# Kernel tuning notes

Measured on AMD Instinct MI355X. Metric: run time of the kernel, lower is better.

## Reference

```python
import jax, jax.numpy as jnp
import numpy as np

N = 50000      # nodes
E = 1600000    # edges
M = 2          # modalities
DIN, H1, LAT, DEC, HID, NC = 2000, 500, 128, 64, 64, 16
EPS = 1e-5


def setup_inputs() -> dict:
    key = jax.random.key(0)
    ks = jax.random.split(key, 24)
    s = 0.02
    return {
        "x": jax.random.normal(ks[0], (M, N, DIN), jnp.float32),
        "src": jax.random.randint(ks[1], (E,), 0, N, jnp.int32),
        "dst": jax.random.randint(ks[2], (E,), 0, N, jnp.int32),
        "W1": jax.random.normal(ks[3], (M, DIN, H1), jnp.float32) * s,
        "b1": jax.random.normal(ks[4], (M, H1), jnp.float32) * s,
        "g1": jax.random.uniform(ks[5], (M, H1), jnp.float32) + 0.5,
        "be1": jax.random.normal(ks[6], (M, H1), jnp.float32) * s,
        "m1": jax.random.normal(ks[7], (M, H1), jnp.float32) * s,
        "v1": jax.random.uniform(ks[8], (M, H1), jnp.float32) + 0.5,
        "W2": jax.random.normal(ks[9], (M, H1, LAT), jnp.float32) * s,
        "b2": jax.random.normal(ks[10], (M, LAT), jnp.float32) * s,
        "g2": jax.random.uniform(ks[11], (M, LAT), jnp.float32) + 0.5,
        "be2": jax.random.normal(ks[12], (M, LAT), jnp.float32) * s,
        "m2": jax.random.normal(ks[13], (M, LAT), jnp.float32) * s,
        "v2": jax.random.uniform(ks[14], (M, LAT), jnp.float32) + 0.5,
        "Wd": jax.random.normal(ks[15], (M, LAT, DEC), jnp.float32) * s,
        "bd": jax.random.normal(ks[16], (M, DEC), jnp.float32) * s,
        "Wg1": jax.random.normal(ks[17], (DEC, HID), jnp.float32) * s,
        "bg1": jax.random.normal(ks[18], (HID,), jnp.float32) * s,
        "Wg2": jax.random.normal(ks[19], (HID, NC), jnp.float32) * s,
        "bg2": jax.random.normal(ks[20], (NC,), jnp.float32) * s,
    }


def _bn(h, g, b, m, v):
    # inference-mode BatchNorm1d; params broadcast over [M, 1, F]
    return (h - m[:, None, :]) * jax.lax.rsqrt(v[:, None, :] + EPS) * g[:, None, :] + b[:, None, :]


def reference(x, src, dst, W1, b1, g1, be1, m1, v1, W2, b2, g2, be2, m2, v2,
              Wd, bd, Wg1, bg1, Wg2, bg2):
    # --- multi-modal encoders (dropout = identity at eval) ---
    h = jnp.einsum('mnd,mdh->mnh', x, W1) + b1[:, None, :]        # [M,N,500]
    h = _bn(h, g1, be1, m1, v1)
    h = jnp.einsum('mnh,mhl->mnl', h, W2) + b2[:, None, :]        # [M,N,LAT]
    h = _bn(h, g2, be2, m2, v2)
    dec = jnp.einsum('mnl,mld->mnd', h, Wd) + bd[:, None, :]      # [M,N,DEC]
    node_features = jnp.mean(dec, axis=0)                         # [N,DEC]

    # --- GraphConv (DGL norm='both'): D_out^{-1/2} on src, D_in^{-1/2} on dst ---
    ones = jnp.ones(src.shape[0], jnp.float32)
    deg_out = jax.ops.segment_sum(ones, src, num_segments=N)
    deg_in = jax.ops.segment_sum(ones, dst, num_segments=N)
    c_src = jax.lax.rsqrt(jnp.clip(deg_out, 1.0))[:, None]
    c_dst = jax.lax.rsqrt(jnp.clip(deg_in, 1.0))[:, None]

    def gconv(feat, W, b):
        msg = (feat * c_src)[src]                                 # [E,F]
        agg = jax.ops.segment_sum(msg, dst, num_segments=N)       # [N,F]
        return (agg * c_dst) @ W + b

    h = jax.nn.relu(gconv(node_features, Wg1, bg1))               # [N,HID]
    score = gconv(h, Wg2, bg2)                                    # [N,NC]
    return score
```

## Files before the change

### kernel.cpp

```cpp
#include <hip/hip_runtime.h>

#define NN 50000
#define EE 1600000
#define MM 2
#define DIN 2000
#define H1 500
#define LAT 128
#define DECF 64
#define KTOT (MM*DIN)
#define KSTEPS (KTOT/32)
#define NTILES (NN/16)
#define EPSBN 1e-5f

typedef float f32x4 __attribute__((ext_vector_type(4)));
typedef short short8v __attribute__((ext_vector_type(8)));

__device__ __forceinline__ unsigned int pkbf(float a, float b){
  unsigned int ua = __float_as_uint(a), ub = __float_as_uint(b);
  ua = (ua + 0x7FFFu + ((ua>>16)&1u)) >> 16;
  ub = (ub + 0x7FFFu + ((ub>>16)&1u)) & 0xFFFF0000u;
  return ua | ub;
}

__global__ __launch_bounds__(256) void prepA(const float* __restrict__ W2,const float* __restrict__ Wd,
                      const float* __restrict__ g2,const float* __restrict__ v2,
                      float* __restrict__ T){
  __shared__ float a2[LAT];
  int m = (blockIdx.x*4) / H1;
  if (threadIdx.x < LAT)
    a2[threadIdx.x] = g2[m*LAT+threadIdx.x]*rsqrtf(v2[m*LAT+threadIdx.x]+EPSBN);
  __syncthreads();
  int g = blockIdx.x*256 + threadIdx.x;
  int d = g & 63; int mk = g >> 6; int k = mk % H1;
  const float* w2 = W2 + (size_t)(m*H1 + k)*LAT;
  const float* wd = Wd + (size_t)m*LAT*DECF + d;
  float acc = 0.f;
  for (int l = 0; l < LAT; ++l) acc += w2[l]*a2[l]*wd[(size_t)l*DECF];
  T[g] = acc;
}

__global__ __launch_bounds__(256) void prepB(const float* __restrict__ W1,const float* __restrict__ g1,
                      const float* __restrict__ v1,const float* __restrict__ T,
                      unsigned short* __restrict__ WB){
  __shared__ float a1[H1];
  int m = (blockIdx.x*4) / DIN;
  for (int k = threadIdx.x; k < H1; k += 256)
    a1[k] = g1[m*H1+k]*rsqrtf(v1[m*H1+k]+EPSBN);
  __syncthreads();
  int g = blockIdx.x*256 + threadIdx.x;
  int d = g & 63; int mi = g >> 6; int i = mi % DIN;
  const float* w1 = W1 + (size_t)(m*DIN + i)*H1;
  const float* t  = T + (size_t)m*H1*DECF + d;
  float acc = 0.f;
  for (int k = 0; k < H1; ++k) acc += w1[k]*a1[k]*t[(size_t)k*DECF];
  acc *= 0.5f;
  unsigned int u = __float_as_uint(acc);
  unsigned short bf = (unsigned short)((u + 0x7FFFu + ((u>>16)&1u)) >> 16);
  int kc = m*DIN + i;
  int s = kc >> 5, kl = kc & 31;
  int laneB = ((kl>>3)<<4) | (d & 15);
  int t4 = d >> 4;
  WB[((size_t)((s*4 + t4)*64 + laneB))*8 + (kl & 7)] = bf;
}

__global__ void prepC(const float* __restrict__ b1,const float* __restrict__ g1,const float* __restrict__ be1,
                      const float* __restrict__ m1,const float* __restrict__ v1,
                      const float* __restrict__ b2,const float* __restrict__ g2,const float* __restrict__ be2,
                      const float* __restrict__ m2,const float* __restrict__ v2,
                      const float* __restrict__ T,const float* __restrict__ Wd,
                      const float* __restrict__ bd, float* __restrict__ cbar){
  __shared__ float part[128];
  int d = threadIdx.x & 63, h = threadIdx.x >> 6;
  float s = 0.f;
  for (int m = 0; m < MM; ++m){
    if (h == 0) s += bd[m*DECF + d];
    const float* t = T + (size_t)m*H1*DECF + d;
    for (int k = h*(H1/2); k < (h+1)*(H1/2); ++k){
      float a = g1[m*H1+k]*rsqrtf(v1[m*H1+k]+EPSBN);
      float c = (b1[m*H1+k]-m1[m*H1+k])*a + be1[m*H1+k];
      s += c*t[(size_t)k*DECF];
    }
    const float* wd = Wd + (size_t)m*LAT*DECF + d;
    for (int l = h*(LAT/2); l < (h+1)*(LAT/2); ++l){
      float a = g2[m*LAT+l]*rsqrtf(v2[m*LAT+l]+EPSBN);
      float c = (b2[m*LAT+l]-m2[m*LAT+l])*a + be2[m*LAT+l];
      s += c*wd[(size_t)l*DECF];
    }
  }
  part[threadIdx.x] = s;
  __syncthreads();
  if (h == 0) cbar[d] = 0.5f*(part[d] + part[64+d]);
}

__global__ void degk(const int* __restrict__ src,const int* __restrict__ dst,
                     int* __restrict__ dout,int* __restrict__ din){
  int e = blockIdx.x*blockDim.x + threadIdx.x;
  if (e >= EE) return;
  atomicAdd(&dout[src[e]], 1);
  atomicAdd(&din[dst[e]], 1);
}

__global__ __launch_bounds__(1024) void scan1(const int* __restrict__ deg, int* __restrict__ rp,
                      int* __restrict__ bsum, int n){
  __shared__ int sm[1024];
  int i = blockIdx.x*1024 + threadIdx.x;
  int v = (i < n) ? deg[i] : 0;
  sm[threadIdx.x] = v; __syncthreads();
  for (int off=1; off<1024; off<<=1){
    int t = (threadIdx.x >= off) ? sm[threadIdx.x-off] : 0;
    __syncthreads();
    sm[threadIdx.x] += t;
    __syncthreads();
  }
  if (i < n) rp[i] = sm[threadIdx.x] - v;
  if (threadIdx.x == 1023) bsum[blockIdx.x] = sm[1023];
}

__global__ void scan3n(int* __restrict__ rp, const int* __restrict__ bsum,
                       const int* __restrict__ dout, const int* __restrict__ din,
                       float* __restrict__ csrc, float* __restrict__ cdst){
  int i = blockIdx.x*blockDim.x + threadIdx.x;
  if (i >= NN) return;
  int b = i >> 10;
  int base = 0;
  for (int j = 0; j < b; ++j) base += bsum[j];
  rp[i] += base;
  if (i == NN-1) rp[NN] = EE;
  int a = dout[i]; if (a < 1) a = 1;
  int dd = din[i]; if (dd < 1) dd = 1;
  csrc[i] = rsqrtf((float)a);
  cdst[i] = rsqrtf((float)dd);
}

__global__ void scatk(const int* __restrict__ src,const int* __restrict__ dst,
                      const int* __restrict__ rp,int* __restrict__ cur,int* __restrict__ ss){
  int e = blockIdx.x*blockDim.x + threadIdx.x;
  if (e >= EE) return;
  int d = dst[e];
  int p = rp[d] + atomicAdd(&cur[d], 1);
  ss[p] = src[e];
}

__global__ __launch_bounds__(256) void gemm_nf(
    const float* __restrict__ x, const short8v* __restrict__ WB,
    const float* __restrict__ cbar, const float* __restrict__ csrc,
    float* __restrict__ nfpre, int* __restrict__ ticket)
{
  const int lane = threadIdx.x & 63;
  const int r = lane & 15;
  const int kg = (lane >> 4) << 3;
  const int rg = (lane >> 4) << 2;
  const float cb0 = cbar[r], cb1 = cbar[16+r], cb2 = cbar[32+r], cb3 = cbar[48+r];

  while (true){
    int t = 0;
    if (lane == 0) t = atomicAdd(ticket, 1);
    t = __shfl(t, 0, 64);
    if (t >= NTILES) break;
    const int n0 = t*16;
    const float* xrow = x + (size_t)(n0 + r) * DIN;

    f32x4 acc0 = {0.f,0.f,0.f,0.f}, acc1 = acc0, acc2 = acc0, acc3 = acc0;
    f32x4 A0c, A1c; short8v B0c, B1c, B2c, B3c;
    {
      const float* p = xrow + kg;
      A0c = *(const f32x4*)p; A1c = *(const f32x4*)(p+4);
      const short8v* bp = WB + lane;
      B0c = bp[0]; B1c = bp[64]; B2c = bp[128]; B3c = bp[192];
    }
    for (int s = 0; s < KSTEPS-1; ++s){
      f32x4 A0n, A1n; short8v B0n, B1n, B2n, B3n;
      {
        int kr = (s+1)*32 + kg;
        const float* p = (kr < DIN) ? (xrow + kr)
                                    : (xrow + (size_t)(NN-1)*DIN + kr);
        A0n = *(const f32x4*)p; A1n = *(const f32x4*)(p+4);
        const short8v* bp = WB + (size_t)(s+1)*256 + lane;
        B0n = bp[0]; B1n = bp[64]; B2n = bp[128]; B3n = bp[192];
      }
      union { short8v v; unsigned int u[4]; } AF;
      AF.u[0]=pkbf(A0c[0],A0c[1]); AF.u[1]=pkbf(A0c[2],A0c[3]);
      AF.u[2]=pkbf(A1c[0],A1c[1]); AF.u[3]=pkbf(A1c[2],A1c[3]);
      acc0 = __builtin_amdgcn_mfma_f32_16x16x32_bf16(AF.v, B0c, acc0, 0,0,0);
      acc1 = __builtin_amdgcn_mfma_f32_16x16x32_bf16(AF.v, B1c, acc1, 0,0,0);
      acc2 = __builtin_amdgcn_mfma_f32_16x16x32_bf16(AF.v, B2c, acc2, 0,0,0);
      acc3 = __builtin_amdgcn_mfma_f32_16x16x32_bf16(AF.v, B3c, acc3, 0,0,0);
      A0c=A0n; A1c=A1n; B0c=B0n; B1c=B1n; B2c=B2n; B3c=B3n;
    }
    {
      union { short8v v; unsigned int u[4]; } AF;
      AF.u[0]=pkbf(A0c[0],A0c[1]); AF.u[1]=pkbf(A0c[2],A0c[3]);
      AF.u[2]=pkbf(A1c[0],A1c[1]); AF.u[3]=pkbf(A1c[2],A1c[3]);
      acc0 = __builtin_amdgcn_mfma_f32_16x16x32_bf16(AF.v, B0c, acc0, 0,0,0);
      acc1 = __builtin_amdgcn_mfma_f32_16x16x32_bf16(AF.v, B1c, acc1, 0,0,0);
      acc2 = __builtin_amdgcn_mfma_f32_16x16x32_bf16(AF.v, B2c, acc2, 0,0,0);
      acc3 = __builtin_amdgcn_mfma_f32_16x16x32_bf16(AF.v, B3c, acc3, 0,0,0);
    }
    #pragma unroll
    for (int rr = 0; rr < 4; ++rr){
      int rowD = n0 + rg + rr;
      float cs = csrc[rowD];
      float* o = nfpre + (size_t)rowD*64 + r;
      o[0]  = (acc0[rr] + cb0)*cs;
      o[16] = (acc1[rr] + cb1)*cs;
      o[32] = (acc2[rr] + cb2)*cs;
      o[48] = (acc3[rr] + cb3)*cs;
    }
  }
}

__global__ __launch_bounds__(512) void fgd1(const float* __restrict__ nf,const int* __restrict__ rp,
                      const int* __restrict__ ss,const float* __restrict__ Wg1,
                      const float* __restrict__ bg1,const float* __restrict__ csrc,
                      const float* __restrict__ cdst,float* __restrict__ hpre){
  __shared__ float W[64*64];
  for (int i = threadIdx.x; i < 64*64; i += 512) W[i] = Wg1[i];
  __syncthreads();
  int wave = threadIdx.x >> 6, lane = threadIdx.x & 63;
  int n = blockIdx.x*8 + wave;
  int q = lane >> 4, c0 = (lane & 15)*4;
  int beg = rp[n], end = rp[n+1];
  f32x4 s4 = {0.f,0.f,0.f,0.f};
  int e = beg + q;
  for (; e + 12 < end; e += 16){
    int i0 = ss[e], i1 = ss[e+4], i2 = ss[e+8], i3 = ss[e+12];
    f32x4 f0 = *(const f32x4*)(nf + (size_t)i0*64 + c0);
    f32x4 f1 = *(const f32x4*)(nf + (size_t)i1*64 + c0);
    f32x4 f2 = *(const f32x4*)(nf + (size_t)i2*64 + c0);
    f32x4 f3 = *(const f32x4*)(nf + (size_t)i3*64 + c0);
    s4 += (f0 + f1) + (f2 + f3);
  }
  for (; e < end; e += 4)
    s4 += *(const f32x4*)(nf + (size_t)ss[e]*64 + c0);
  s4.x += __shfl_xor(s4.x,16); s4.y += __shfl_xor(s4.y,16);
  s4.z += __shfl_xor(s4.z,16); s4.w += __shfl_xor(s4.w,16);
  s4.x += __shfl_xor(s4.x,32); s4.y += __shfl_xor(s4.y,32);
  s4.z += __shfl_xor(s4.z,32); s4.w += __shfl_xor(s4.w,32);
  float acc = 0.f;
  #pragma unroll
  for (int l16 = 0; l16 < 16; ++l16){
    acc += __shfl(s4.x,l16) * W[(4*l16+0)*64 + lane];
    acc += __shfl(s4.y,l16) * W[(4*l16+1)*64 + lane];
    acc += __shfl(s4.z,l16) * W[(4*l16+2)*64 + lane];
    acc += __shfl(s4.w,l16) * W[(4*l16+3)*64 + lane];
  }
  float h = fmaxf(cdst[n]*acc + bg1[lane], 0.f) * csrc[n];
  hpre[(size_t)n*64 + lane] = h;
}

__global__ __launch_bounds__(512) void fgd2(const float* __restrict__ hp,const int* __restrict__ rp,
                      const int* __restrict__ ss,const float* __restrict__ Wg2,
                      const float* __restrict__ bg2,const float* __restrict__ cdst,
                      float* __restrict__ score){
  __shared__ float W[64*16];
  for (int i = threadIdx.x; i < 64*16; i += 512) W[i] = Wg2[i];
  __syncthreads();
  int wave = threadIdx.x >> 6, lane = threadIdx.x & 63;
  int n = blockIdx.x*8 + wave;
  int q = lane >> 4, c0 = (lane & 15)*4;
  int beg = rp[n], end = rp[n+1];
  f32x4 s4 = {0.f,0.f,0.f,0.f};
  int e = beg + q;
  for (; e + 12 < end; e += 16){
    int i0 = ss[e], i1 = ss[e+4], i2 = ss[e+8], i3 = ss[e+12];
    f32x4 f0 = *(const f32x4*)(hp + (size_t)i0*64 + c0);
    f32x4 f1 = *(const f32x4*)(hp + (size_t)i1*64 + c0);
    f32x4 f2 = *(const f32x4*)(hp + (size_t)i2*64 + c0);
    f32x4 f3 = *(const f32x4*)(hp + (size_t)i3*64 + c0);
    s4 += (f0 + f1) + (f2 + f3);
  }
  for (; e < end; e += 4)
    s4 += *(const f32x4*)(hp + (size_t)ss[e]*64 + c0);
  s4.x += __shfl_xor(s4.x,16); s4.y += __shfl_xor(s4.y,16);
  s4.z += __shfl_xor(s4.z,16); s4.w += __shfl_xor(s4.w,16);
  s4.x += __shfl_xor(s4.x,32); s4.y += __shfl_xor(s4.y,32);
  s4.z += __shfl_xor(s4.z,32); s4.w += __shfl_xor(s4.w,32);
  int c = lane & 15;
  float acc = 0.f;
  #pragma unroll
  for (int l16 = 0; l16 < 16; ++l16){
    acc += __shfl(s4.x,l16) * W[(4*l16+0)*16 + c];
    acc += __shfl(s4.y,l16) * W[(4*l16+1)*16 + c];
    acc += __shfl(s4.z,l16) * W[(4*l16+2)*16 + c];
    acc += __shfl(s4.w,l16) * W[(4*l16+3)*16 + c];
  }
  if (lane < 16) score[(size_t)n*16 + lane] = cdst[n]*acc + bg2[lane];
}

extern "C" void kernel_launch(void* const* d_in, const int* in_sizes, int n_in,
                              void* d_out, int out_size, void* d_ws, size_t ws_size,
                              hipStream_t stream){
  const float* x   = (const float*)d_in[0];
  const int* src   = (const int*)d_in[1];
  const int* dst   = (const int*)d_in[2];
  const float* W1  = (const float*)d_in[3];
  const float* b1  = (const float*)d_in[4];
  const float* g1  = (const float*)d_in[5];
  const float* be1 = (const float*)d_in[6];
  const float* m1  = (const float*)d_in[7];
  const float* v1  = (const float*)d_in[8];
  const float* W2  = (const float*)d_in[9];
  const float* b2  = (const float*)d_in[10];
  const float* g2  = (const float*)d_in[11];
  const float* be2 = (const float*)d_in[12];
  const float* m2  = (const float*)d_in[13];
  const float* v2  = (const float*)d_in[14];
  const float* Wd  = (const float*)d_in[15];
  const float* bd  = (const float*)d_in[16];
  const float* Wg1 = (const float*)d_in[17];
  const float* bg1 = (const float*)d_in[18];
  const float* Wg2 = (const float*)d_in[19];
  const float* bg2 = (const float*)d_in[20];
  float* score = (float*)d_out;

  char* w = (char*)d_ws;
  size_t off = 0;
  auto alc = [&](size_t b){ size_t c = off; off += (b + 255) & ~(size_t)255; return c; };
  size_t o_dout = alc((size_t)NN*4), o_din = alc((size_t)NN*4), o_cur = alc((size_t)NN*4);
  size_t o_tick = alc(256);
  size_t zspan = off;
  size_t o_rp  = alc((size_t)(NN+1)*4), o_bsum = alc(256*4);
  size_t o_csrc = alc((size_t)NN*4), o_cdst = alc((size_t)NN*4);
  size_t o_T = alc((size_t)MM*H1*DECF*4), o_cbar = alc(DECF*4);
  size_t o_WB = alc((size_t)MM*DIN*DECF*2);
  size_t o_ss = alc((size_t)EE*4);
  size_t o_nf = alc((size_t)NN*64*4);
  size_t o_hp = alc((size_t)NN*64*4);

  int* dout = (int*)(w+o_dout); int* din = (int*)(w+o_din); int* cur = (int*)(w+o_cur);
  int* tick = (int*)(w+o_tick);
  int* rp = (int*)(w+o_rp); int* bsum = (int*)(w+o_bsum);
  float* csrc = (float*)(w+o_csrc); float* cdst = (float*)(w+o_cdst);
  float* T = (float*)(w+o_T); float* cbar = (float*)(w+o_cbar);
  unsigned short* WBu = (unsigned short*)(w+o_WB);
  int* ss = (int*)(w+o_ss);
  float* nf = (float*)(w+o_nf); float* hp = (float*)(w+o_hp);

  hipMemsetAsync(w, 0, zspan, stream);

  prepA<<<(MM*H1*DECF)/256,256,0,stream>>>(W2,Wd,g2,v2,T);
  prepB<<<(MM*DIN*DECF)/256,256,0,stream>>>(W1,g1,v1,T,WBu);
  prepC<<<1,128,0,stream>>>(b1,g1,be1,m1,v1,b2,g2,be2,m2,v2,T,Wd,bd,cbar);

  degk<<<(EE+255)/256,256,0,stream>>>(src,dst,dout,din);
  int nb = (NN+1023)/1024;
  scan1<<<nb,1024,0,stream>>>(din,rp,bsum,NN);
  scan3n<<<(NN+255)/256,256,0,stream>>>(rp,bsum,dout,din,csrc,cdst);
  scatk<<<(EE+255)/256,256,0,stream>>>(src,dst,rp,cur,ss);

  gemm_nf<<<768,256,0,stream>>>(x,(const short8v*)(w+o_WB),cbar,csrc,nf,tick);

  fgd1<<<NN/8,512,0,stream>>>(nf,rp,ss,Wg1,bg1,csrc,cdst,hp);
  fgd2<<<NN/8,512,0,stream>>>(hp,rp,ss,Wg2,bg2,cdst,score);
}
```

Baseline: 797.4 us.

## Fuse degree counting into GEMM launch, store node features as bf16, persistent gconv

```diff
diff --git a/kernel.cpp b/kernel.cpp
--- a/kernel.cpp
+++ b/kernel.cpp
@@ -10,10 +10,13 @@
 #define KTOT (MM*DIN)
 #define KSTEPS (KTOT/32)
 #define NTILES (NN/16)
+#define GEMM_BLKS 768
+#define DEG_BLKS 256
 #define EPSBN 1e-5f
 
 typedef float f32x4 __attribute__((ext_vector_type(4)));
 typedef short short8v __attribute__((ext_vector_type(8)));
+typedef unsigned int u32x2 __attribute__((ext_vector_type(2)));
 
 __device__ __forceinline__ unsigned int pkbf(float a, float b){
   unsigned int ua = __float_as_uint(a), ub = __float_as_uint(b);
@@ -21,6 +24,12 @@
   ub = (ub + 0x7FFFu + ((ub>>16)&1u)) & 0xFFFF0000u;
   return ua | ub;
 }
+__device__ __forceinline__ unsigned short pk1(float a){
+  unsigned int u = __float_as_uint(a);
+  return (unsigned short)((u + 0x7FFFu + ((u>>16)&1u)) >> 16);
+}
+__device__ __forceinline__ float bfe0(unsigned int w){ return __uint_as_float(w<<16); }
+__device__ __forceinline__ float bfe1(unsigned int w){ return __uint_as_float(w & 0xFFFF0000u); }
 
 __global__ __launch_bounds__(256) void prepA(const float* __restrict__ W2,const float* __restrict__ Wd,
                       const float* __restrict__ g2,const float* __restrict__ v2,
@@ -92,14 +101,6 @@
   if (h == 0) cbar[d] = 0.5f*(part[d] + part[64+d]);
 }
 
-__global__ void degk(const int* __restrict__ src,const int* __restrict__ dst,
-                     int* __restrict__ dout,int* __restrict__ din){
-  int e = blockIdx.x*blockDim.x + threadIdx.x;
-  if (e >= EE) return;
-  atomicAdd(&dout[src[e]], 1);
-  atomicAdd(&din[dst[e]], 1);
-}
-
 __global__ __launch_bounds__(1024) void scan1(const int* __restrict__ deg, int* __restrict__ rp,
                       int* __restrict__ bsum, int n){
   __shared__ int sm[1024];
@@ -141,11 +142,21 @@
   ss[p] = src[e];
 }
 
-__global__ __launch_bounds__(256) void gemm_nf(
+__global__ __launch_bounds__(256,4) void gemm_deg(
     const float* __restrict__ x, const short8v* __restrict__ WB,
-    const float* __restrict__ cbar, const float* __restrict__ csrc,
-    float* __restrict__ nfpre, int* __restrict__ ticket)
+    const float* __restrict__ cbar,
+    unsigned short* __restrict__ nfb, int* __restrict__ ticket,
+    const int* __restrict__ src, const int* __restrict__ dst,
+    int* __restrict__ dout, int* __restrict__ din)
 {
+  if (blockIdx.x >= GEMM_BLKS){
+    int t0 = (blockIdx.x - GEMM_BLKS)*256 + threadIdx.x;
+    for (int e = t0; e < EE; e += 256*DEG_BLKS){
+      atomicAdd(&dout[src[e]], 1);
+      atomicAdd(&din[dst[e]], 1);
+    }
+    return;
+  }
   const int lane = threadIdx.x & 63;
   const int r = lane & 15;
   const int kg = (lane >> 4) << 3;
@@ -199,92 +210,110 @@
     #pragma unroll
     for (int rr = 0; rr < 4; ++rr){
       int rowD = n0 + rg + rr;
-      float cs = csrc[rowD];
-      float* o = nfpre + (size_t)rowD*64 + r;
-      o[0]  = (acc0[rr] + cb0)*cs;
-      o[16] = (acc1[rr] + cb1)*cs;
-      o[32] = (acc2[rr] + cb2)*cs;
-      o[48] = (acc3[rr] + cb3)*cs;
-    }
-  }
-}
-
-__global__ __launch_bounds__(512) void fgd1(const float* __restrict__ nf,const int* __restrict__ rp,
-                      const int* __restrict__ ss,const float* __restrict__ Wg1,
-                      const float* __restrict__ bg1,const float* __restrict__ csrc,
-                      const float* __restrict__ cdst,float* __restrict__ hpre){
+      unsigned short* o = nfb + (size_t)rowD*64 + r;
+      o[0]  = pk1(acc0[rr] + cb0);
+      o[16] = pk1(acc1[rr] + cb1);
+      o[32] = pk1(acc2[rr] + cb2);
+      o[48] = pk1(acc3[rr] + cb3);
+    }
+  }
+}
+
+__global__ __launch_bounds__(512,4) void fgd1(const unsigned short* __restrict__ nfb,
+                      const int* __restrict__ rp,const int* __restrict__ ss,
+                      const float* __restrict__ Wg1,const float* __restrict__ bg1,
+                      const float* __restrict__ csrc,const float* __restrict__ cdst,
+                      unsigned short* __restrict__ hpb){
   __shared__ float W[64*64];
   for (int i = threadIdx.x; i < 64*64; i += 512) W[i] = Wg1[i];
   __syncthreads();
   int wave = threadIdx.x >> 6, lane = threadIdx.x & 63;
-  int n = blockIdx.x*8 + wave;
-  int q = lane >> 4, c0 = (lane & 15)*4;
-  int beg = rp[n], end = rp[n+1];
-  f32x4 s4 = {0.f,0.f,0.f,0.f};
-  int e = beg + q;
-  for (; e + 12 < end; e += 16){
-    int i0 = ss[e], i1 = ss[e+4], i2 = ss[e+8], i3 = ss[e+12];
-    f32x4 f0 = *(const f32x4*)(nf + (size_t)i0*64 + c0);
-    f32x4 f1 = *(const f32x4*)(nf + (size_t)i1*64 + c0);
-    f32x4 f2 = *(const f32x4*)(nf + (size_t)i2*64 + c0);
-    f32x4 f3 = *(const f32x4*)(nf + (size_t)i3*64 + c0);
-    s4 += (f0 + f1) + (f2 + f3);
-  }
-  for (; e < end; e += 4)
-    s4 += *(const f32x4*)(nf + (size_t)ss[e]*64 + c0);
-  s4.x += __shfl_xor(s4.x,16); s4.y += __shfl_xor(s4.y,16);
-  s4.z += __shfl_xor(s4.z,16); s4.w += __shfl_xor(s4.w,16);
-  s4.x += __shfl_xor(s4.x,32); s4.y += __shfl_xor(s4.y,32);
-  s4.z += __shfl_xor(s4.z,32); s4.w += __shfl_xor(s4.w,32);
-  float acc = 0.f;
-  #pragma unroll
-  for (int l16 = 0; l16 < 16; ++l16){
-    acc += __shfl(s4.x,l16) * W[(4*l16+0)*64 + lane];
-    acc += __shfl(s4.y,l16) * W[(4*l16+1)*64 + lane];
-    acc += __shfl(s4.z,l16) * W[(4*l16+2)*64 + lane];
-    acc += __shfl(s4.w,l16) * W[(4*l16+3)*64 + lane];
-  }
-  float h = fmaxf(cdst[n]*acc + bg1[lane], 0.f) * csrc[n];
-  hpre[(size_t)n*64 + lane] = h;
-}
-
-__global__ __launch_bounds__(512) void fgd2(const float* __restrict__ hp,const int* __restrict__ rp,
-                      const int* __restrict__ ss,const float* __restrict__ Wg2,
-                      const float* __restrict__ bg2,const float* __restrict__ cdst,
-                      float* __restrict__ score){
+  int q = lane >> 4, cc = (lane & 15)*4;
+  const int NW = 512*8;
+  for (int n = blockIdx.x*8 + wave; n < NN; n += NW){
+    int beg = rp[n], end = rp[n+1];
+    f32x4 s4 = {0.f,0.f,0.f,0.f};
+    int e = beg + q;
+    for (; e + 12 < end; e += 16){
+      int i0 = ss[e], i1 = ss[e+4], i2 = ss[e+8], i3 = ss[e+12];
+      float c0 = csrc[i0], c1 = csrc[i1], c2 = csrc[i2], c3 = csrc[i3];
+      u32x2 w0 = *(const u32x2*)(nfb + (size_t)i0*64 + cc);
+      u32x2 w1 = *(const u32x2*)(nfb + (size_t)i1*64 + cc);
+      u32x2 w2 = *(const u32x2*)(nfb + (size_t)i2*64 + cc);
+      u32x2 w3 = *(const u32x2*)(nfb + (size_t)i3*64 + cc);
+      s4.x += c0*bfe0(w0.x) + c1*bfe0(w1.x) + c2*bfe0(w2.x) + c3*bfe0(w3.x);
+      s4.y += c0*bfe1(w0.x) + c1*bfe1(w1.x) + c2*bfe1(w2.x) + c3*bfe1(w3.x);
+      s4.z += c0*bfe0(w0.y) + c1*bfe0(w1.y) + c2*bfe0(w2.y) + c3*bfe0(w3.y);
+      s4.w += c0*bfe1(w0.y) + c1*bfe1(w1.y) + c2*bfe1(w2.y) + c3*bfe1(w3.y);
+    }
+    for (; e < end; e += 4){
+      int i0 = ss[e]; float c0 = csrc[i0];
+      u32x2 w0 = *(const u32x2*)(nfb + (size_t)i0*64 + cc);
+      s4.x += c0*bfe0(w0.x); s4.y += c0*bfe1(w0.x);
+      s4.z += c0*bfe0(w0.y); s4.w += c0*bfe1(w0.y);
+    }
+    s4.x += __shfl_xor(s4.x,16); s4.y += __shfl_xor(s4.y,16);
+    s4.z += __shfl_xor(s4.z,16); s4.w += __shfl_xor(s4.w,16);
+    s4.x += __shfl_xor(s4.x,32); s4.y += __shfl_xor(s4.y,32);
+    s4.z += __shfl_xor(s4.z,32); s4.w += __shfl_xor(s4.w,32);
+    float acc = 0.f;
+    #pragma unroll
+    for (int l16 = 0; l16 < 16; ++l16){
+      acc += __shfl(s4.x,l16) * W[(4*l16+0)*64 + lane];
+      acc += __shfl(s4.y,l16) * W[(4*l16+1)*64 + lane];
+      acc += __shfl(s4.z,l16) * W[(4*l16+2)*64 + lane];
+      acc += __shfl(s4.w,l16) * W[(4*l16+3)*64 + lane];
+    }
+    float h = fmaxf(cdst[n]*acc + bg1[lane], 0.f) * csrc[n];
+    hpb[(size_t)n*64 + lane] = pk1(h);
+  }
+}
+
+__global__ __launch_bounds__(512,4) void fgd2(const unsigned short* __restrict__ hpb,
+                      const int* __restrict__ rp,const int* __restrict__ ss,
+                      const float* __restrict__ Wg2,const float* __restrict__ bg2,
+                      const float* __restrict__ cdst,float* __restrict__ score){
   __shared__ float W[64*16];
   for (int i = threadIdx.x; i < 64*16; i += 512) W[i] = Wg2[i];
   __syncthreads();
   int wave = threadIdx.x >> 6, lane = threadIdx.x & 63;
-  int n = blockIdx.x*8 + wave;
-  int q = lane >> 4, c0 = (lane & 15)*4;
-  int beg = rp[n], end = rp[n+1];
-  f32x4 s4 = {0.f,0.f,0.f,0.f};
-  int e = beg + q;
-  for (; e + 12 < end; e += 16){
-    int i0 = ss[e], i1 = ss[e+4], i2 = ss[e+8], i3 = ss[e+12];
-    f32x4 f0 = *(const f32x4*)(hp + (size_t)i0*64 + c0);
-    f32x4 f1 = *(const f32x4*)(hp + (size_t)i1*64 + c0);
-    f32x4 f2 = *(const f32x4*)(hp + (size_t)i2*64 + c0);
-    f32x4 f3 = *(const f32x4*)(hp + (size_t)i3*64 + c0);
-    s4 += (f0 + f1) + (f2 + f3);
-  }
-  for (; e < end; e += 4)
-    s4 += *(const f32x4*)(hp + (size_t)ss[e]*64 + c0);
-  s4.x += __shfl_xor(s4.x,16); s4.y += __shfl_xor(s4.y,16);
-  s4.z += __shfl_xor(s4.z,16); s4.w += __shfl_xor(s4.w,16);
-  s4.x += __shfl_xor(s4.x,32); s4.y += __shfl_xor(s4.y,32);
-  s4.z += __shfl_xor(s4.z,32); s4.w += __shfl_xor(s4.w,32);
-  int c = lane & 15;
-  float acc = 0.f;
-  #pragma unroll
-  for (int l16 = 0; l16 < 16; ++l16){
-    acc += __shfl(s4.x,l16) * W[(4*l16+0)*16 + c];
-    acc += __shfl(s4.y,l16) * W[(4*l16+1)*16 + c];
-    acc += __shfl(s4.z,l16) * W[(4*l16+2)*16 + c];
-    acc += __shfl(s4.w,l16) * W[(4*l16+3)*16 + c];
-  }
-  if (lane < 16) score[(size_t)n*16 + lane] = cdst[n]*acc + bg2[lane];
+  int q = lane >> 4, cc = (lane & 15)*4;
+  const int NW = 512*8;
+  for (int n = blockIdx.x*8 + wave; n < NN; n += NW){
+    int beg = rp[n], end = rp[n+1];
+    f32x4 s4 = {0.f,0.f,0.f,0.f};
+    int e = beg + q;
+    for (; e + 12 < end; e += 16){
+      int i0 = ss[e], i1 = ss[e+4], i2 = ss[e+8], i3 = ss[e+12];
+      u32x2 w0 = *(const u32x2*)(hpb + (size_t)i0*64 + cc);
+      u32x2 w1 = *(const u32x2*)(hpb + (size_t)i1*64 + cc);
+      u32x2 w2 = *(const u32x2*)(hpb + (size_t)i2*64 + cc);
+      u32x2 w3 = *(const u32x2*)(hpb + (size_t)i3*64 + cc);
+      s4.x += bfe0(w0.x) + bfe0(w1.x) + bfe0(w2.x) + bfe0(w3.x);
+      s4.y += bfe1(w0.x) + bfe1(w1.x) + bfe1(w2.x) + bfe1(w3.x);
+      s4.z += bfe0(w0.y) + bfe0(w1.y) + bfe0(w2.y) + bfe0(w3.y);
+      s4.w += bfe1(w0.y) + bfe1(w1.y) + bfe1(w2.y) + bfe1(w3.y);
+    }
+    for (; e < end; e += 4){
+      u32x2 w0 = *(const u32x2*)(hpb + (size_t)ss[e]*64 + cc);
+      s4.x += bfe0(w0.x); s4.y += bfe1(w0.x);
+      s4.z += bfe0(w0.y); s4.w += bfe1(w0.y);
+    }
+    s4.x += __shfl_xor(s4.x,16); s4.y += __shfl_xor(s4.y,16);
+    s4.z += __shfl_xor(s4.z,16); s4.w += __shfl_xor(s4.w,16);
+    s4.x += __shfl_xor(s4.x,32); s4.y += __shfl_xor(s4.y,32);
+    s4.z += __shfl_xor(s4.z,32); s4.w += __shfl_xor(s4.w,32);
+    int c = lane & 15;
+    float acc = 0.f;
+    #pragma unroll
+    for (int l16 = 0; l16 < 16; ++l16){
+      acc += __shfl(s4.x,l16) * W[(4*l16+0)*16 + c];
+      acc += __shfl(s4.y,l16) * W[(4*l16+1)*16 + c];
+      acc += __shfl(s4.z,l16) * W[(4*l16+2)*16 + c];
+      acc += __shfl(s4.w,l16) * W[(4*l16+3)*16 + c];
+    }
+    if (lane < 16) score[(size_t)n*16 + lane] = cdst[n]*acc + bg2[lane];
+  }
 }
 
 extern "C" void kernel_launch(void* const* d_in, const int* in_sizes, int n_in,
@@ -324,8 +353,8 @@
   size_t o_T = alc((size_t)MM*H1*DECF*4), o_cbar = alc(DECF*4);
   size_t o_WB = alc((size_t)MM*DIN*DECF*2);
   size_t o_ss = alc((size_t)EE*4);
-  size_t o_nf = alc((size_t)NN*64*4);
-  size_t o_hp = alc((size_t)NN*64*4);
+  size_t o_nf = alc((size_t)NN*64*2);
+  size_t o_hp = alc((size_t)NN*64*2);
 
   int* dout = (int*)(w+o_dout); int* din = (int*)(w+o_din); int* cur = (int*)(w+o_cur);
   int* tick = (int*)(w+o_tick);
@@ -334,7 +363,8 @@
   float* T = (float*)(w+o_T); float* cbar = (float*)(w+o_cbar);
   unsigned short* WBu = (unsigned short*)(w+o_WB);
   int* ss = (int*)(w+o_ss);
-  float* nf = (float*)(w+o_nf); float* hp = (float*)(w+o_hp);
+  unsigned short* nfb = (unsigned short*)(w+o_nf);
+  unsigned short* hpb = (unsigned short*)(w+o_hp);
 
   hipMemsetAsync(w, 0, zspan, stream);
 
@@ -342,14 +372,14 @@
   prepB<<<(MM*DIN*DECF)/256,256,0,stream>>>(W1,g1,v1,T,WBu);
   prepC<<<1,128,0,stream>>>(b1,g1,be1,m1,v1,b2,g2,be2,m2,v2,T,Wd,bd,cbar);
 
-  degk<<<(EE+255)/256,256,0,stream>>>(src,dst,dout,din);
+  gemm_deg<<<GEMM_BLKS+DEG_BLKS,256,0,stream>>>(x,(const short8v*)(w+o_WB),cbar,
+                                                nfb,tick,src,dst,dout,din);
+
   int nb = (NN+1023)/1024;
   scan1<<<nb,1024,0,stream>>>(din,rp,bsum,NN);
   scan3n<<<(NN+255)/256,256,0,stream>>>(rp,bsum,dout,din,csrc,cdst);
   scatk<<<(EE+255)/256,256,0,stream>>>(src,dst,rp,cur,ss);
 
-  gemm_nf<<<768,256,0,stream>>>(x,(const short8v*)(w+o_WB),cbar,csrc,nf,tick);
-
-  fgd1<<<NN/8,512,0,stream>>>(nf,rp,ss,Wg1,bg1,csrc,cdst,hp);
-  fgd2<<<NN/8,512,0,stream>>>(hp,rp,ss,Wg2,bg2,cdst,score);
-}
+  fgd1<<<512,512,0,stream>>>(nfb,rp,ss,Wg1,bg1,csrc,cdst,hpb);
+  fgd2<<<512,512,0,stream>>>(hpb,rp,ss,Wg2,bg2,cdst,score);
+}
```

Measured after the change: 702.7 us. -11.9%, faster.
